# Kernel optimization log

Measured on AMD Instinct MI355X. Metric: run time of the kernel, lower is better.

Reference implementation:

```python
import jax, jax.numpy as jnp
import numpy as np

E = 256        # emb_size
H = 8          # num_heads
D = E // H     # head_dim = 32
FF = 3 * E     # 768
NE = 6         # num_experts
TOPK = 2
EPS = 1e-6


def rotate_half(x):
    x1 = x[..., ::2]
    x2 = x[..., 1::2]
    return jnp.stack((-x2, x1), axis=-1).reshape(x.shape)


def rope_cos_sin(seq_len):
    inv_freq = 1.0 / (10000.0 ** (jnp.arange(0, D, 2, dtype=jnp.float32) / D))
    pos = jnp.arange(seq_len, dtype=jnp.float32)
    freqs = jnp.outer(pos, inv_freq)              # [S, D/2]
    emb = jnp.concatenate([freqs, freqs], axis=-1)  # [S, D]
    return jnp.cos(emb)[None, None], jnp.sin(emb)[None, None]


def rmsnorm(x, w):
    rms = jax.lax.rsqrt(jnp.mean(x * x, axis=-1, keepdims=True) + EPS)
    return x * rms * w


def setup_inputs() -> dict:
    key = jax.random.key(0)
    ks = jax.random.split(key, 10)
    s = lambda fan_in: 1.0 / np.sqrt(fan_in)
    return {
        "x": jax.random.normal(ks[0], (4, 2048, E), dtype=jnp.float32),
        "Wqkv": jax.random.uniform(ks[1], (E, 3 * E), jnp.float32, -s(E), s(E)),
        "Wout": jax.random.uniform(ks[2], (E, E), jnp.float32, -s(E), s(E)),
        "rms1_w": jnp.ones((E,), jnp.float32),
        "rms2_w": jnp.ones((E,), jnp.float32),
        "gate_W": jax.random.uniform(ks[3], (E, NE), jnp.float32, -s(E), s(E)),
        "Wg": jax.random.uniform(ks[4], (NE, E, FF), jnp.float32, -s(E), s(E)),
        "Wu": jax.random.uniform(ks[5], (NE, E, FF), jnp.float32, -s(E), s(E)),
        "Wd": jax.random.uniform(ks[6], (NE, FF, E), jnp.float32, -s(FF), s(FF)),
    }


def attention(xn, Wqkv, Wout):
    B, S, _ = xn.shape
    qkv = (xn @ Wqkv).reshape(B, S, 3, H, D).transpose(2, 0, 3, 1, 4)  # [3,B,H,S,D]
    q, k, v = qkv[0], qkv[1], qkv[2]
    cos, sin = rope_cos_sin(S)
    q = q * cos + rotate_half(q) * sin
    k = k * cos + rotate_half(k) * sin
    scores = jnp.einsum("bhqd,bhkd->bhqk", q, k) * (D ** -0.5)
    causal = jnp.arange(S)[None, :] > jnp.arange(S)[:, None]
    scores = jnp.where(causal[None, None], -jnp.inf, scores)
    attn = jax.nn.softmax(scores, axis=-1)
    out = jnp.einsum("bhqk,bhkd->bhqd", attn, v)
    out = out.transpose(0, 2, 1, 3).reshape(B, S, E)
    return out @ Wout


def moe(xn, gate_W, Wg, Wu, Wd):
    B, S, _ = xn.shape
    N = B * S
    gate_weights = jax.nn.softmax(xn @ gate_W, axis=-1)          # [B,S,NE]
    topk_w, topk_i = jax.lax.top_k(gate_weights, TOPK)           # [B,S,K]
    topk_w = jax.nn.softmax(topk_w, axis=-1)
    xf = xn.reshape(N, E)
    idx = topk_i.reshape(N, TOPK)
    wts = topk_w.reshape(N, TOPK)
    # dense all-expert compute, as in the original
    expert_out = jnp.einsum("ntf,nfe->nte",
                            jax.nn.silu(jnp.einsum("te,nef->ntf", xf, Wg))
                            * jnp.einsum("te,nef->ntf", xf, Wu),
                            Wd)                                   # [NE, N, E]
    weighted_sel = jnp.zeros((N, NE), xf.dtype).at[jnp.arange(N)[:, None], idx].add(wts)
    out = jnp.einsum("nte,tn->te", expert_out, weighted_sel).reshape(B, S, E)
    # load balancing aux loss
    importance = gate_weights.mean(axis=(0, 1))                   # [NE]
    load = jnp.zeros((NE,), xf.dtype).at[idx.reshape(-1)].add(1.0) / N
    aux_loss = NE * jnp.sum(importance * load)
    return out, aux_loss


def reference(x, Wqkv, Wout, rms1_w, rms2_w, gate_W, Wg, Wu, Wd):
    attn_out = attention(rmsnorm(x, rms1_w), Wqkv, Wout)
    x = x + attn_out
    ff_out, aux_loss = moe(rmsnorm(x, rms2_w), gate_W, Wg, Wu, Wd)
    return x + ff_out, aux_loss
```

## Files before the change

kernel.cpp:

```cpp
#include <hip/hip_runtime.h>
#include <hip/hip_bf16.h>
#include <math.h>

#define NE 6

typedef __bf16 bf16x8 __attribute__((ext_vector_type(8)));
typedef float f32x4 __attribute__((ext_vector_type(4)));
typedef short short8 __attribute__((ext_vector_type(8)));

#define SWZ(row, kbyte) (((row) * 128) + ((kbyte) ^ (((row) & 7) << 4)))

static __device__ __forceinline__ short f2bf(float f) {
    __hip_bfloat16 h = __float2bfloat16(f);
    return __builtin_bit_cast(short, h);
}

static __device__ __forceinline__ float bf2f(short s) {
    return __bfloat162float(__builtin_bit_cast(__hip_bfloat16, s));
}

__global__ void rope_tables(float* __restrict__ ct, float* __restrict__ st) {
    int id = blockIdx.x * 256 + threadIdx.x;
    if (id >= 2048 * 16) return;
    int s = id >> 4, f = id & 15;
    float invf = expf(-logf(10000.0f) * (float)f / 16.0f);
    float ang = (float)s * invf;
    ct[id] = cosf(ang);
    st[id] = sinf(ang);
}

__global__ void rmsnorm_k(const float* __restrict__ x, const float* __restrict__ w,
                          float* __restrict__ o) {
    __shared__ float red[256];
    int n = blockIdx.x, t = threadIdx.x;
    float v = x[n * 256 + t];
    red[t] = v * v;
    __syncthreads();
    for (int s = 128; s > 0; s >>= 1) {
        if (t < s) red[t] += red[t + s];
        __syncthreads();
    }
    float rms = rsqrtf(red[0] / 256.0f + 1e-6f);
    o[n * 256 + t] = v * rms * w[t];
}

__global__ void rmsnorm_both(const float* __restrict__ x, const float* __restrict__ w,
                             float* __restrict__ o, short* __restrict__ obf) {
    __shared__ float red[256];
    int n = blockIdx.x, t = threadIdx.x;
    float v = x[n * 256 + t];
    red[t] = v * v;
    __syncthreads();
    for (int s = 128; s > 0; s >>= 1) {
        if (t < s) red[t] += red[t + s];
        __syncthreads();
    }
    float rms = rsqrtf(red[0] / 256.0f + 1e-6f);
    float val = v * rms * w[t];
    o[n * 256 + t] = val;
    obf[n * 256 + t] = f2bf(val);
}

__global__ __launch_bounds__(256) void transcvt_k(const float* __restrict__ src,
                                                  short* __restrict__ dst, int R, int C) {
    __shared__ short tile[32][33];
    const float* s = src + (size_t)blockIdx.z * R * C;
    short* d = dst + (size_t)blockIdx.z * R * C;
    int t = threadIdx.x;
    int c0 = blockIdx.x * 32, r0 = blockIdx.y * 32;
    int ci = t & 31, ri0 = t >> 5;
#pragma unroll
    for (int it = 0; it < 4; it++) {
        int ri = ri0 + it * 8;
        tile[ri][ci] = f2bf(s[(size_t)(r0 + ri) * C + c0 + ci]);
    }
    __syncthreads();
#pragma unroll
    for (int it = 0; it < 4; it++) {
        int rj = ri0 + it * 8;
        d[(size_t)(c0 + rj) * R + r0 + ci] = tile[ci][rj];
    }
}

__global__ __launch_bounds__(256) void gemm_qkv(const float* __restrict__ A,
                                                const float* __restrict__ W,
                                                float* __restrict__ Q, float* __restrict__ Kq,
                                                float* __restrict__ V) {
    __shared__ float As[16][64];
    __shared__ float Bs[16][64];
    int t = threadIdx.x;
    int m0 = blockIdx.y * 64, n0 = blockIdx.x * 64;
    float acc[4][4] = {};
    int am = t >> 2, ak = (t & 3) * 4;
    int bk = t >> 4, bn = (t & 15) * 4;
    int tm = (t & 15) * 4, tn = (t >> 4) * 4;
    for (int k0 = 0; k0 < 256; k0 += 16) {
        float4 av = *(const float4*)&A[(m0 + am) * 256 + k0 + ak];
        As[ak + 0][am] = av.x; As[ak + 1][am] = av.y; As[ak + 2][am] = av.z; As[ak + 3][am] = av.w;
        float4 bv = *(const float4*)&W[(k0 + bk) * 768 + n0 + bn];
        *(float4*)&Bs[bk][bn] = bv;
        __syncthreads();
#pragma unroll
        for (int kk = 0; kk < 16; kk++) {
            float4 a4 = *(float4*)&As[kk][tm];
            float4 b4 = *(float4*)&Bs[kk][tn];
            float a[4] = {a4.x, a4.y, a4.z, a4.w};
            float b[4] = {b4.x, b4.y, b4.z, b4.w};
#pragma unroll
            for (int i = 0; i < 4; i++)
#pragma unroll
                for (int j = 0; j < 4; j++) acc[i][j] += a[i] * b[j];
        }
        __syncthreads();
    }
    int part = n0 >> 8;
    float* dst = part == 0 ? Q : (part == 1 ? Kq : V);
#pragma unroll
    for (int i = 0; i < 4; i++) {
        int rowi = m0 + tm + i;
        int b = rowi >> 11, s = rowi & 2047;
#pragma unroll
        for (int j = 0; j < 4; j++) {
            int c = n0 + tn + j;
            int e = c & 255, h = e >> 5, d = e & 31;
            dst[(((size_t)(b * 8 + h)) * 2048 + s) * 32 + d] = acc[i][j];
        }
    }
}

__global__ void rope_k(float* __restrict__ Q, float* __restrict__ Kq,
                       const float* __restrict__ ct, const float* __restrict__ st) {
    int id = blockIdx.x * 256 + threadIdx.x;
    if (id >= 32 * 2048 * 16) return;
    int i = id & 15;
    int s = (id >> 4) & 2047;
    int bh = id >> 15;
    int base = (bh * 2048 + s) * 32 + 2 * i;
    int j0 = (2 * i) & 15;
    float c0 = ct[s * 16 + j0], s0 = st[s * 16 + j0];
    float c1 = ct[s * 16 + j0 + 1], s1 = st[s * 16 + j0 + 1];
    float2 q = *(float2*)&Q[base];
    float2 k = *(float2*)&Kq[base];
    float2 qo, ko;
    qo.x = q.x * c0 - q.y * s0;
    qo.y = q.y * c1 + q.x * s1;
    ko.x = k.x * c0 - k.y * s0;
    ko.y = k.y * c1 + k.x * s1;
    *(float2*)&Q[base] = qo;
    *(float2*)&Kq[base] = ko;
}

__global__ __launch_bounds__(256) void attn_k(const float* __restrict__ Q,
                                              const float* __restrict__ Kg,
                                              const float* __restrict__ Vg,
                                              float* __restrict__ ctx) {
    __shared__ float4 Kl[64][8];
    __shared__ float4 Vl[64][8];
    int bh = blockIdx.x;
    int qt = gridDim.y - 1 - blockIdx.y;
    int t = threadIdx.x;
    int sub = t & 3;
    int row = qt * 64 + (t >> 2);
    const float4* Qb = (const float4*)(Q + (size_t)bh * 2048 * 32);
    const float4* Kb = (const float4*)(Kg + (size_t)bh * 2048 * 32);
    const float4* Vb = (const float4*)(Vg + (size_t)bh * 2048 * 32);
    float4 q0 = Qb[row * 8 + sub * 2];
    float4 q1 = Qb[row * 8 + sub * 2 + 1];
    float4 o0 = {}, o1 = {};
    float m = -1e30f, l = 0.f;
    const float scale = 0.17677669529663687f;
    int ntile = qt + 1;
    float4* Klf = &Kl[0][0];
    float4* Vlf = &Vl[0][0];
    for (int kt = 0; kt < ntile; kt++) {
        int kbase = kt * 64;
        Klf[t] = Kb[kbase * 8 + t];
        Klf[t + 256] = Kb[kbase * 8 + t + 256];
        Vlf[t] = Vb[kbase * 8 + t];
        Vlf[t + 256] = Vb[kbase * 8 + t + 256];
        __syncthreads();
        int jmax = row - kbase + 1;
        if (jmax > 64) jmax = 64;
        for (int j = 0; j < jmax; j++) {
            float4 k0 = Kl[j][sub * 2];
            float4 k1 = Kl[j][sub * 2 + 1];
            float s = q0.x * k0.x + q0.y * k0.y + q0.z * k0.z + q0.w * k0.w +
                      q1.x * k1.x + q1.y * k1.y + q1.z * k1.z + q1.w * k1.w;
            s += __shfl_xor(s, 1);
            s += __shfl_xor(s, 2);
            s *= scale;
            if (s > m) {
                float r = __expf(m - s);
                o0.x *= r; o0.y *= r; o0.z *= r; o0.w *= r;
                o1.x *= r; o1.y *= r; o1.z *= r; o1.w *= r;
                l *= r;
                m = s;
            }
            float p = __expf(s - m);
            l += p;
            float4 v0 = Vl[j][sub * 2];
            float4 v1 = Vl[j][sub * 2 + 1];
            o0.x += p * v0.x; o0.y += p * v0.y; o0.z += p * v0.z; o0.w += p * v0.w;
            o1.x += p * v1.x; o1.y += p * v1.y; o1.z += p * v1.z; o1.w += p * v1.w;
        }
        __syncthreads();
    }
    float invl = 1.f / l;
    int b = bh >> 3, h = bh & 7;
    float4* cp = (float4*)(ctx + ((size_t)(b * 2048 + row)) * 256 + h * 32 + sub * 8);
    o0.x *= invl; o0.y *= invl; o0.z *= invl; o0.w *= invl;
    o1.x *= invl; o1.y *= invl; o1.z *= invl; o1.w *= invl;
    cp[0] = o0;
    cp[1] = o1;
}

__global__ __launch_bounds__(256) void gemm_out(const float* __restrict__ A,
                                                const float* __restrict__ W,
                                                const float* __restrict__ xres,
                                                float* __restrict__ x2) {
    __shared__ float As[16][64];
    __shared__ float Bs[16][64];
    int t = threadIdx.x;
    int m0 = blockIdx.y * 64, n0 = blockIdx.x * 64;
    float acc[4][4] = {};
    int am = t >> 2, ak = (t & 3) * 4;
    int bk = t >> 4, bn = (t & 15) * 4;
    int tm = (t & 15) * 4, tn = (t >> 4) * 4;
    for (int k0 = 0; k0 < 256; k0 += 16) {
        float4 av = *(const float4*)&A[(m0 + am) * 256 + k0 + ak];
        As[ak + 0][am] = av.x; As[ak + 1][am] = av.y; As[ak + 2][am] = av.z; As[ak + 3][am] = av.w;
        float4 bv = *(const float4*)&W[(k0 + bk) * 256 + n0 + bn];
        *(float4*)&Bs[bk][bn] = bv;
        __syncthreads();
#pragma unroll
        for (int kk = 0; kk < 16; kk++) {
            float4 a4 = *(float4*)&As[kk][tm];
            float4 b4 = *(float4*)&Bs[kk][tn];
            float a[4] = {a4.x, a4.y, a4.z, a4.w};
            float b[4] = {b4.x, b4.y, b4.z, b4.w};
#pragma unroll
            for (int i = 0; i < 4; i++)
#pragma unroll
                for (int j = 0; j < 4; j++) acc[i][j] += a[i] * b[j];
        }
        __syncthreads();
    }
#pragma unroll
    for (int i = 0; i < 4; i++) {
        int rowi = m0 + tm + i;
#pragma unroll
        for (int j = 0; j < 4; j++) {
            int c = n0 + tn + j;
            x2[rowi * 256 + c] = acc[i][j] + xres[rowi * 256 + c];
        }
    }
}

__global__ void gate_k(const float* __restrict__ xn2, const float* __restrict__ gw,
                       int* __restrict__ idx, float* __restrict__ wts,
                       int* __restrict__ cnt, float* __restrict__ imp) {
    __shared__ float simp[NE];
    __shared__ int scnt[NE];
    int t = threadIdx.x;
    int n = blockIdx.x * 256 + t;
    if (t < NE) { simp[t] = 0.f; scnt[t] = 0; }
    __syncthreads();
    float lg[NE] = {0, 0, 0, 0, 0, 0};
    for (int k = 0; k < 256; k++) {
        float xv = xn2[n * 256 + k];
#pragma unroll
        for (int e = 0; e < NE; e++) lg[e] += xv * gw[k * NE + e];
    }
    float mx = lg[0];
#pragma unroll
    for (int e = 1; e < NE; e++) mx = fmaxf(mx, lg[e]);
    float p[NE], se = 0.f;
#pragma unroll
    for (int e = 0; e < NE; e++) { p[e] = expf(lg[e] - mx); se += p[e]; }
    float inv = 1.f / se;
#pragma unroll
    for (int e = 0; e < NE; e++) p[e] *= inv;
    int i1 = 0; float v1 = p[0];
#pragma unroll
    for (int e = 1; e < NE; e++) if (p[e] > v1) { v1 = p[e]; i1 = e; }
    int i2 = -1; float v2 = -1.f;
#pragma unroll
    for (int e = 0; e < NE; e++) if (e != i1 && p[e] > v2) { v2 = p[e]; i2 = e; }
    float e2v = expf(v2 - v1);
    float w1 = 1.f / (1.f + e2v);
    float w2 = e2v / (1.f + e2v);
    idx[n * 2] = i1; idx[n * 2 + 1] = i2;
    wts[n * 2] = w1; wts[n * 2 + 1] = w2;
#pragma unroll
    for (int e = 0; e < NE; e++) atomicAdd(&simp[e], p[e]);
    atomicAdd(&scnt[i1], 1);
    atomicAdd(&scnt[i2], 1);
    __syncthreads();
    if (t < NE) {
        atomicAdd(&imp[t], simp[t]);
        atomicAdd(&cnt[t], scnt[t]);
    }
}

__global__ void prefix_k(const int* __restrict__ cnt, const float* __restrict__ imp,
                         int* __restrict__ offs, int* __restrict__ cur,
                         float* __restrict__ auxout) {
    if (threadIdx.x == 0) {
        int o = 0;
        float a = 0.f;
        for (int e = 0; e < NE; e++) {
            offs[e] = o;
            cur[e] = o;
            o += cnt[e];
            a += imp[e] * (float)cnt[e];
        }
        auxout[0] = 6.0f * a / (8192.0f * 8192.0f);
    }
}

__global__ void scatter_k(const int* __restrict__ idx, int* __restrict__ cur,
                          int* __restrict__ ltok, int* __restrict__ slotp) {
    int n = blockIdx.x * 256 + threadIdx.x;
#pragma unroll
    for (int s = 0; s < 2; s++) {
        int e = idx[n * 2 + s];
        int pos = atomicAdd(&cur[e], 1);
        ltok[pos] = n;
        slotp[n * 2 + s] = pos;
    }
}

__global__ __launch_bounds__(256) void mfma_moe1(const short* __restrict__ xnbf,
                                                 const short* __restrict__ WgT,
                                                 const short* __restrict__ WuT,
                                                 const int* __restrict__ cnt,
                                                 const int* __restrict__ offs,
                                                 const int* __restrict__ ltok,
                                                 short* __restrict__ Hbuf) {
    int e = blockIdx.z;
    int Me = cnt[e];
    int m0 = blockIdx.y * 64;
    if (m0 >= Me) return;
    int off = offs[e];
    __shared__ short As[4096], Bg[4096], Bu[4096];
    __shared__ int stok[64];
    int t = threadIdx.x;
    if (t < 64) stok[t] = (m0 + t < Me) ? ltok[off + m0 + t] : ltok[off];
    __syncthreads();
    int n0 = blockIdx.x * 64;
    const short* WgE = WgT + (size_t)e * 768 * 256;
    const short* WuE = WuT + (size_t)e * 768 * 256;
    int lane = t & 63, wid = t >> 6, wr = wid >> 1, wc = wid & 1;
    int l15 = lane & 15, lh = lane >> 4;
    int r = t >> 3, k8 = (t & 7) * 8, kb8 = (t & 7) * 16;
    char* AsC = (char*)As; char* BgC = (char*)Bg; char* BuC = (char*)Bu;
    f32x4 accg[2][2] = {}, accu[2][2] = {};
    for (int k0 = 0; k0 < 256; k0 += 64) {
        short8 av0 = *(const short8*)&xnbf[(size_t)stok[r] * 256 + k0 + k8];
        short8 av1 = *(const short8*)&xnbf[(size_t)stok[r + 32] * 256 + k0 + k8];
        short8 gv0 = *(const short8*)&WgE[(size_t)(n0 + r) * 256 + k0 + k8];
        short8 gv1 = *(const short8*)&WgE[(size_t)(n0 + r + 32) * 256 + k0 + k8];
        short8 uv0 = *(const short8*)&WuE[(size_t)(n0 + r) * 256 + k0 + k8];
        short8 uv1 = *(const short8*)&WuE[(size_t)(n0 + r + 32) * 256 + k0 + k8];
        *(short8*)(AsC + SWZ(r, kb8)) = av0;
        *(short8*)(AsC + SWZ(r + 32, kb8)) = av1;
        *(short8*)(BgC + SWZ(r, kb8)) = gv0;
        *(short8*)(BgC + SWZ(r + 32, kb8)) = gv1;
        *(short8*)(BuC + SWZ(r, kb8)) = uv0;
        *(short8*)(BuC + SWZ(r + 32, kb8)) = uv1;
        __syncthreads();
#pragma unroll
        for (int kk = 0; kk < 2; kk++) {
            int kb = kk * 64 + lh * 16;
            bf16x8 a[2], bg[2], bu[2];
#pragma unroll
            for (int i = 0; i < 2; i++) {
                a[i]  = *(const bf16x8*)(AsC + SWZ(wr * 32 + i * 16 + l15, kb));
                bg[i] = *(const bf16x8*)(BgC + SWZ(wc * 32 + i * 16 + l15, kb));
                bu[i] = *(const bf16x8*)(BuC + SWZ(wc * 32 + i * 16 + l15, kb));
            }
#pragma unroll
            for (int mi = 0; mi < 2; mi++)
#pragma unroll
                for (int ni = 0; ni < 2; ni++) {
                    accg[mi][ni] = __builtin_amdgcn_mfma_f32_16x16x32_bf16(a[mi], bg[ni], accg[mi][ni], 0, 0, 0);
                    accu[mi][ni] = __builtin_amdgcn_mfma_f32_16x16x32_bf16(a[mi], bu[ni], accu[mi][ni], 0, 0, 0);
                }
        }
        __syncthreads();
    }
#pragma unroll
    for (int mi = 0; mi < 2; mi++)
#pragma unroll
        for (int j = 0; j < 4; j++) {
            int m = m0 + wr * 32 + mi * 16 + lh * 4 + j;
            if (m < Me) {
                size_t rp = (size_t)(off + m) * 768;
#pragma unroll
                for (int ni = 0; ni < 2; ni++) {
                    int c = n0 + wc * 32 + ni * 16 + l15;
                    float g = accg[mi][ni][j], u = accu[mi][ni][j];
                    Hbuf[rp + c] = f2bf(g / (1.f + __expf(-g)) * u);
                }
            }
        }
}

__global__ __launch_bounds__(256) void mfma_moe2(const short* __restrict__ Hbuf,
                                                 const short* __restrict__ WdT,
                                                 const int* __restrict__ cnt,
                                                 const int* __restrict__ offs,
                                                 short* __restrict__ Y) {
    int e = blockIdx.z;
    int Me = cnt[e];
    int m0 = blockIdx.y * 64;
    if (m0 >= Me) return;
    int off = offs[e];
    __shared__ short As[4096], Bs[4096];
    int t = threadIdx.x;
    int n0 = blockIdx.x * 64;
    const short* WdE = WdT + (size_t)e * 256 * 768;
    int lane = t & 63, wid = t >> 6, wr = wid >> 1, wc = wid & 1;
    int l15 = lane & 15, lh = lane >> 4;
    int r = t >> 3, k8 = (t & 7) * 8, kb8 = (t & 7) * 16;
    int ar0 = off + m0 + r;       if (ar0 > 16383) ar0 = 16383;
    int ar1 = off + m0 + r + 32;  if (ar1 > 16383) ar1 = 16383;
    char* AsC = (char*)As; char* BsC = (char*)Bs;
    f32x4 acc[2][2] = {};
    for (int k0 = 0; k0 < 768; k0 += 64) {
        short8 av0 = *(const short8*)&Hbuf[(size_t)ar0 * 768 + k0 + k8];
        short8 av1 = *(const short8*)&Hbuf[(size_t)ar1 * 768 + k0 + k8];
        short8 bv0 = *(const short8*)&WdE[(size_t)(n0 + r) * 768 + k0 + k8];
        short8 bv1 = *(const short8*)&WdE[(size_t)(n0 + r + 32) * 768 + k0 + k8];
        *(short8*)(AsC + SWZ(r, kb8)) = av0;
        *(short8*)(AsC + SWZ(r + 32, kb8)) = av1;
        *(short8*)(BsC + SWZ(r, kb8)) = bv0;
        *(short8*)(BsC + SWZ(r + 32, kb8)) = bv1;
        __syncthreads();
#pragma unroll
        for (int kk = 0; kk < 2; kk++) {
            int kb = kk * 64 + lh * 16;
            bf16x8 a[2], b[2];
#pragma unroll
            for (int i = 0; i < 2; i++) {
                a[i] = *(const bf16x8*)(AsC + SWZ(wr * 32 + i * 16 + l15, kb));
                b[i] = *(const bf16x8*)(BsC + SWZ(wc * 32 + i * 16 + l15, kb));
            }
#pragma unroll
            for (int mi = 0; mi < 2; mi++)
#pragma unroll
                for (int ni = 0; ni < 2; ni++)
                    acc[mi][ni] = __builtin_amdgcn_mfma_f32_16x16x32_bf16(a[mi], b[ni], acc[mi][ni], 0, 0, 0);
        }
        __syncthreads();
    }
#pragma unroll
    for (int mi = 0; mi < 2; mi++)
#pragma unroll
        for (int j = 0; j < 4; j++) {
            int m = m0 + wr * 32 + mi * 16 + lh * 4 + j;
            if (m < Me) {
                size_t rp = (size_t)(off + m) * 256;
#pragma unroll
                for (int ni = 0; ni < 2; ni++) {
                    int c = n0 + wc * 32 + ni * 16 + l15;
                    Y[rp + c] = f2bf(acc[mi][ni][j]);
                }
            }
        }
}

__global__ void combine_k(const float* __restrict__ x2, const short* __restrict__ Y,
                          const int* __restrict__ slotp, const float* __restrict__ wts,
                          float* __restrict__ out) {
    int n = blockIdx.x, t = threadIdx.x;
    int p0 = slotp[n * 2], p1 = slotp[n * 2 + 1];
    float w0 = wts[n * 2], w1 = wts[n * 2 + 1];
    out[n * 256 + t] = x2[n * 256 + t] + w0 * bf2f(Y[(size_t)p0 * 256 + t]) +
                       w1 * bf2f(Y[(size_t)p1 * 256 + t]);
}

extern "C" void kernel_launch(void* const* d_in, const int* in_sizes, int n_in,
                              void* d_out, int out_size, void* d_ws, size_t ws_size,
                              hipStream_t stream) {
    const float* x     = (const float*)d_in[0];
    const float* Wqkv  = (const float*)d_in[1];
    const float* Wout  = (const float*)d_in[2];
    const float* rms1w = (const float*)d_in[3];
    const float* rms2w = (const float*)d_in[4];
    const float* gateW = (const float*)d_in[5];
    const float* Wg    = (const float*)d_in[6];
    const float* Wu    = (const float*)d_in[7];
    const float* Wd    = (const float*)d_in[8];
    float* out = (float*)d_out;
    char* ws = (char*)d_ws;

    float* xn1   = (float*)(ws + 0);
    short* xn2bf = (short*)(ws + 0);
    float* Qb  = (float*)(ws + 8388608);
    float* Kb  = (float*)(ws + 16777216);
    float* Vb  = (float*)(ws + 25165824);
    short* Hbuf = (short*)(ws + 4194304);
    float* ctx = (float*)(ws + 33554432);
    short* WgT = (short*)(ws + 33554432);
    short* WuT = (short*)(ws + 35913728);
    short* WdT = (short*)(ws + 38273024);
    float* x2  = (float*)(ws + 41943040);
    float* xn2 = (float*)(ws + 50331648);
    short* Ybuf = (short*)(ws + 50331648);
    float* ct  = (float*)(ws + 58720256);
    float* st  = (float*)(ws + 58851328);
    int*   idx = (int*)(ws + 58982400);
    float* wts = (float*)(ws + 59047936);
    int* slotp = (int*)(ws + 59113472);
    int* ltok  = (int*)(ws + 59179008);
    int* cnt   = (int*)(ws + 59244544);
    int* offs  = cnt + 8;
    int* cur   = cnt + 16;
    float* imp = (float*)(cnt + 24);

    (void)hipMemsetAsync(cnt, 0, 128, stream);

    rope_tables<<<128, 256, 0, stream>>>(ct, st);
    rmsnorm_k<<<8192, 256, 0, stream>>>(x, rms1w, xn1);
    gemm_qkv<<<dim3(12, 128), 256, 0, stream>>>(xn1, Wqkv, Qb, Kb, Vb);
    rope_k<<<4096, 256, 0, stream>>>(Qb, Kb, ct, st);
    attn_k<<<dim3(32, 32), 256, 0, stream>>>(Qb, Kb, Vb, ctx);
    gemm_out<<<dim3(4, 128), 256, 0, stream>>>(ctx, Wout, x, x2);
    transcvt_k<<<dim3(24, 8, NE), 256, 0, stream>>>(Wg, WgT, 256, 768);
    transcvt_k<<<dim3(24, 8, NE), 256, 0, stream>>>(Wu, WuT, 256, 768);
    transcvt_k<<<dim3(8, 24, NE), 256, 0, stream>>>(Wd, WdT, 768, 256);
    rmsnorm_both<<<8192, 256, 0, stream>>>(x2, rms2w, xn2, xn2bf);
    gate_k<<<32, 256, 0, stream>>>(xn2, gateW, idx, wts, cnt, imp);
    prefix_k<<<1, 64, 0, stream>>>(cnt, imp, offs, cur, out + 2097152);
    scatter_k<<<32, 256, 0, stream>>>(idx, cur, ltok, slotp);
    mfma_moe1<<<dim3(12, 256, NE), 256, 0, stream>>>(xn2bf, WgT, WuT, cnt, offs, ltok, Hbuf);
    mfma_moe2<<<dim3(4, 256, NE), 256, 0, stream>>>(Hbuf, WdT, cnt, offs, Ybuf);
    combine_k<<<8192, 256, 0, stream>>>(x2, Ybuf, slotp, wts, out);
}
```

Measured before the change: 736.0 us.

## Use split-bf16 MFMA for QKV/out GEMMs and unroll attention inner loop by four

```diff
diff --git a/kernel.cpp b/kernel.cpp
--- a/kernel.cpp
+++ b/kernel.cpp
@@ -17,6 +17,11 @@
 
 static __device__ __forceinline__ float bf2f(short s) {
     return __bfloat162float(__builtin_bit_cast(__hip_bfloat16, s));
+}
+
+static __device__ __forceinline__ float dot8(float4 a0, float4 a1, float4 b0, float4 b1) {
+    return a0.x * b0.x + a0.y * b0.y + a0.z * b0.z + a0.w * b0.w +
+           a1.x * b1.x + a1.y * b1.y + a1.z * b1.z + a1.w * b1.w;
 }
 
 __global__ void rope_tables(float* __restrict__ ct, float* __restrict__ st) {
@@ -29,8 +34,8 @@
     st[id] = sinf(ang);
 }
 
-__global__ void rmsnorm_k(const float* __restrict__ x, const float* __restrict__ w,
-                          float* __restrict__ o) {
+__global__ void rmsnorm_hilo(const float* __restrict__ x, const float* __restrict__ w,
+                             short* __restrict__ ohi, short* __restrict__ olo) {
     __shared__ float red[256];
     int n = blockIdx.x, t = threadIdx.x;
     float v = x[n * 256 + t];
@@ -41,7 +46,10 @@
         __syncthreads();
     }
     float rms = rsqrtf(red[0] / 256.0f + 1e-6f);
-    o[n * 256 + t] = v * rms * w[t];
+    float val = v * rms * w[t];
+    short h = f2bf(val);
+    ohi[n * 256 + t] = h;
+    olo[n * 256 + t] = f2bf(val - bf2f(h));
 }
 
 __global__ void rmsnorm_both(const float* __restrict__ x, const float* __restrict__ w,
@@ -82,50 +90,167 @@
     }
 }
 
-__global__ __launch_bounds__(256) void gemm_qkv(const float* __restrict__ A,
-                                                const float* __restrict__ W,
-                                                float* __restrict__ Q, float* __restrict__ Kq,
-                                                float* __restrict__ V) {
-    __shared__ float As[16][64];
-    __shared__ float Bs[16][64];
+__global__ __launch_bounds__(256) void transcvt2_k(const float* __restrict__ src,
+                                                   short* __restrict__ dhi,
+                                                   short* __restrict__ dlo, int R, int C) {
+    __shared__ short th[32][33];
+    __shared__ short tl[32][33];
+    int t = threadIdx.x;
+    int c0 = blockIdx.x * 32, r0 = blockIdx.y * 32;
+    int ci = t & 31, ri0 = t >> 5;
+#pragma unroll
+    for (int it = 0; it < 4; it++) {
+        int ri = ri0 + it * 8;
+        float v = src[(size_t)(r0 + ri) * C + c0 + ci];
+        short h = f2bf(v);
+        th[ri][ci] = h;
+        tl[ri][ci] = f2bf(v - bf2f(h));
+    }
+    __syncthreads();
+#pragma unroll
+    for (int it = 0; it < 4; it++) {
+        int rj = ri0 + it * 8;
+        dhi[(size_t)(c0 + rj) * R + r0 + ci] = th[ci][rj];
+        dlo[(size_t)(c0 + rj) * R + r0 + ci] = tl[ci][rj];
+    }
+}
+
+__global__ __launch_bounds__(256) void mfma_qkv3(const short* __restrict__ Ahi,
+                                                 const short* __restrict__ Alo,
+                                                 const short* __restrict__ Bhi,
+                                                 const short* __restrict__ Blo,
+                                                 float* __restrict__ Q, float* __restrict__ Kq,
+                                                 float* __restrict__ V) {
+    __shared__ short sAh[4096], sAl[4096], sBh[4096], sBl[4096];
     int t = threadIdx.x;
     int m0 = blockIdx.y * 64, n0 = blockIdx.x * 64;
-    float acc[4][4] = {};
-    int am = t >> 2, ak = (t & 3) * 4;
-    int bk = t >> 4, bn = (t & 15) * 4;
-    int tm = (t & 15) * 4, tn = (t >> 4) * 4;
-    for (int k0 = 0; k0 < 256; k0 += 16) {
-        float4 av = *(const float4*)&A[(m0 + am) * 256 + k0 + ak];
-        As[ak + 0][am] = av.x; As[ak + 1][am] = av.y; As[ak + 2][am] = av.z; As[ak + 3][am] = av.w;
-        float4 bv = *(const float4*)&W[(k0 + bk) * 768 + n0 + bn];
-        *(float4*)&Bs[bk][bn] = bv;
-        __syncthreads();
-#pragma unroll
-        for (int kk = 0; kk < 16; kk++) {
-            float4 a4 = *(float4*)&As[kk][tm];
-            float4 b4 = *(float4*)&Bs[kk][tn];
-            float a[4] = {a4.x, a4.y, a4.z, a4.w};
-            float b[4] = {b4.x, b4.y, b4.z, b4.w};
-#pragma unroll
-            for (int i = 0; i < 4; i++)
-#pragma unroll
-                for (int j = 0; j < 4; j++) acc[i][j] += a[i] * b[j];
+    int lane = t & 63, wid = t >> 6, wr = wid >> 1, wc = wid & 1;
+    int l15 = lane & 15, lh = lane >> 4;
+    int r = t >> 3, k8 = (t & 7) * 8, kb8 = (t & 7) * 16;
+    char* Ah = (char*)sAh; char* Al = (char*)sAl; char* Bh = (char*)sBh; char* Bl = (char*)sBl;
+    f32x4 acc[2][2] = {};
+    for (int k0 = 0; k0 < 256; k0 += 64) {
+        short8 ah0 = *(const short8*)&Ahi[(size_t)(m0 + r) * 256 + k0 + k8];
+        short8 ah1 = *(const short8*)&Ahi[(size_t)(m0 + r + 32) * 256 + k0 + k8];
+        short8 al0 = *(const short8*)&Alo[(size_t)(m0 + r) * 256 + k0 + k8];
+        short8 al1 = *(const short8*)&Alo[(size_t)(m0 + r + 32) * 256 + k0 + k8];
+        short8 bh0 = *(const short8*)&Bhi[(size_t)(n0 + r) * 256 + k0 + k8];
+        short8 bh1 = *(const short8*)&Bhi[(size_t)(n0 + r + 32) * 256 + k0 + k8];
+        short8 bl0 = *(const short8*)&Blo[(size_t)(n0 + r) * 256 + k0 + k8];
+        short8 bl1 = *(const short8*)&Blo[(size_t)(n0 + r + 32) * 256 + k0 + k8];
+        *(short8*)(Ah + SWZ(r, kb8)) = ah0;
+        *(short8*)(Ah + SWZ(r + 32, kb8)) = ah1;
+        *(short8*)(Al + SWZ(r, kb8)) = al0;
+        *(short8*)(Al + SWZ(r + 32, kb8)) = al1;
+        *(short8*)(Bh + SWZ(r, kb8)) = bh0;
+        *(short8*)(Bh + SWZ(r + 32, kb8)) = bh1;
+        *(short8*)(Bl + SWZ(r, kb8)) = bl0;
+        *(short8*)(Bl + SWZ(r + 32, kb8)) = bl1;
+        __syncthreads();
+#pragma unroll
+        for (int kk = 0; kk < 2; kk++) {
+            int kb = kk * 64 + lh * 16;
+            bf16x8 ah[2], al[2], bh[2], bl[2];
+#pragma unroll
+            for (int i = 0; i < 2; i++) {
+                ah[i] = *(const bf16x8*)(Ah + SWZ(wr * 32 + i * 16 + l15, kb));
+                al[i] = *(const bf16x8*)(Al + SWZ(wr * 32 + i * 16 + l15, kb));
+                bh[i] = *(const bf16x8*)(Bh + SWZ(wc * 32 + i * 16 + l15, kb));
+                bl[i] = *(const bf16x8*)(Bl + SWZ(wc * 32 + i * 16 + l15, kb));
+            }
+#pragma unroll
+            for (int mi = 0; mi < 2; mi++)
+#pragma unroll
+                for (int ni = 0; ni < 2; ni++) {
+                    acc[mi][ni] = __builtin_amdgcn_mfma_f32_16x16x32_bf16(ah[mi], bh[ni], acc[mi][ni], 0, 0, 0);
+                    acc[mi][ni] = __builtin_amdgcn_mfma_f32_16x16x32_bf16(ah[mi], bl[ni], acc[mi][ni], 0, 0, 0);
+                    acc[mi][ni] = __builtin_amdgcn_mfma_f32_16x16x32_bf16(al[mi], bh[ni], acc[mi][ni], 0, 0, 0);
+                }
         }
         __syncthreads();
     }
     int part = n0 >> 8;
     float* dst = part == 0 ? Q : (part == 1 ? Kq : V);
 #pragma unroll
-    for (int i = 0; i < 4; i++) {
-        int rowi = m0 + tm + i;
-        int b = rowi >> 11, s = rowi & 2047;
+    for (int mi = 0; mi < 2; mi++)
 #pragma unroll
         for (int j = 0; j < 4; j++) {
-            int c = n0 + tn + j;
-            int e = c & 255, h = e >> 5, d = e & 31;
-            dst[(((size_t)(b * 8 + h)) * 2048 + s) * 32 + d] = acc[i][j];
-        }
-    }
+            int m = m0 + wr * 32 + mi * 16 + lh * 4 + j;
+            int b = m >> 11, s = m & 2047;
+#pragma unroll
+            for (int ni = 0; ni < 2; ni++) {
+                int c = n0 + wc * 32 + ni * 16 + l15;
+                int e = c & 255, h = e >> 5, d = e & 31;
+                dst[(((size_t)(b * 8 + h)) * 2048 + s) * 32 + d] = acc[mi][ni][j];
+            }
+        }
+}
+
+__global__ __launch_bounds__(256) void mfma_out3(const short* __restrict__ Ahi,
+                                                 const short* __restrict__ Alo,
+                                                 const short* __restrict__ Bhi,
+                                                 const short* __restrict__ Blo,
+                                                 const float* __restrict__ xres,
+                                                 float* __restrict__ x2) {
+    __shared__ short sAh[4096], sAl[4096], sBh[4096], sBl[4096];
+    int t = threadIdx.x;
+    int m0 = blockIdx.y * 64, n0 = blockIdx.x * 64;
+    int lane = t & 63, wid = t >> 6, wr = wid >> 1, wc = wid & 1;
+    int l15 = lane & 15, lh = lane >> 4;
+    int r = t >> 3, k8 = (t & 7) * 8, kb8 = (t & 7) * 16;
+    char* Ah = (char*)sAh; char* Al = (char*)sAl; char* Bh = (char*)sBh; char* Bl = (char*)sBl;
+    f32x4 acc[2][2] = {};
+    for (int k0 = 0; k0 < 256; k0 += 64) {
+        short8 ah0 = *(const short8*)&Ahi[(size_t)(m0 + r) * 256 + k0 + k8];
+        short8 ah1 = *(const short8*)&Ahi[(size_t)(m0 + r + 32) * 256 + k0 + k8];
+        short8 al0 = *(const short8*)&Alo[(size_t)(m0 + r) * 256 + k0 + k8];
+        short8 al1 = *(const short8*)&Alo[(size_t)(m0 + r + 32) * 256 + k0 + k8];
+        short8 bh0 = *(const short8*)&Bhi[(size_t)(n0 + r) * 256 + k0 + k8];
+        short8 bh1 = *(const short8*)&Bhi[(size_t)(n0 + r + 32) * 256 + k0 + k8];
+        short8 bl0 = *(const short8*)&Blo[(size_t)(n0 + r) * 256 + k0 + k8];
+        short8 bl1 = *(const short8*)&Blo[(size_t)(n0 + r + 32) * 256 + k0 + k8];
+        *(short8*)(Ah + SWZ(r, kb8)) = ah0;
+        *(short8*)(Ah + SWZ(r + 32, kb8)) = ah1;
+        *(short8*)(Al + SWZ(r, kb8)) = al0;
+        *(short8*)(Al + SWZ(r + 32, kb8)) = al1;
+        *(short8*)(Bh + SWZ(r, kb8)) = bh0;
+        *(short8*)(Bh + SWZ(r + 32, kb8)) = bh1;
+        *(short8*)(Bl + SWZ(r, kb8)) = bl0;
+        *(short8*)(Bl + SWZ(r + 32, kb8)) = bl1;
+        __syncthreads();
+#pragma unroll
+        for (int kk = 0; kk < 2; kk++) {
+            int kb = kk * 64 + lh * 16;
+            bf16x8 ah[2], al[2], bh[2], bl[2];
+#pragma unroll
+            for (int i = 0; i < 2; i++) {
+                ah[i] = *(const bf16x8*)(Ah + SWZ(wr * 32 + i * 16 + l15, kb));
+                al[i] = *(const bf16x8*)(Al + SWZ(wr * 32 + i * 16 + l15, kb));
+                bh[i] = *(const bf16x8*)(Bh + SWZ(wc * 32 + i * 16 + l15, kb));
+                bl[i] = *(const bf16x8*)(Bl + SWZ(wc * 32 + i * 16 + l15, kb));
+            }
+#pragma unroll
+            for (int mi = 0; mi < 2; mi++)
+#pragma unroll
+                for (int ni = 0; ni < 2; ni++) {
+                    acc[mi][ni] = __builtin_amdgcn_mfma_f32_16x16x32_bf16(ah[mi], bh[ni], acc[mi][ni], 0, 0, 0);
+                    acc[mi][ni] = __builtin_amdgcn_mfma_f32_16x16x32_bf16(ah[mi], bl[ni], acc[mi][ni], 0, 0, 0);
+                    acc[mi][ni] = __builtin_amdgcn_mfma_f32_16x16x32_bf16(al[mi], bh[ni], acc[mi][ni], 0, 0, 0);
+                }
+        }
+        __syncthreads();
+    }
+#pragma unroll
+    for (int mi = 0; mi < 2; mi++)
+#pragma unroll
+        for (int j = 0; j < 4; j++) {
+            int m = m0 + wr * 32 + mi * 16 + lh * 4 + j;
+#pragma unroll
+            for (int ni = 0; ni < 2; ni++) {
+                int c = n0 + wc * 32 + ni * 16 + l15;
+                x2[(size_t)m * 256 + c] = acc[mi][ni][j] + xres[(size_t)m * 256 + c];
+            }
+        }
 }
 
 __global__ void rope_k(float* __restrict__ Q, float* __restrict__ Kq,
@@ -153,7 +278,8 @@
 __global__ __launch_bounds__(256) void attn_k(const float* __restrict__ Q,
                                               const float* __restrict__ Kg,
                                               const float* __restrict__ Vg,
-                                              float* __restrict__ ctx) {
+                                              short* __restrict__ ctxh,
+                                              short* __restrict__ ctxl) {
     __shared__ float4 Kl[64][8];
     __shared__ float4 Vl[64][8];
     int bh = blockIdx.x;
@@ -181,79 +307,64 @@
         __syncthreads();
         int jmax = row - kbase + 1;
         if (jmax > 64) jmax = 64;
-        for (int j = 0; j < jmax; j++) {
-            float4 k0 = Kl[j][sub * 2];
-            float4 k1 = Kl[j][sub * 2 + 1];
-            float s = q0.x * k0.x + q0.y * k0.y + q0.z * k0.z + q0.w * k0.w +
-                      q1.x * k1.x + q1.y * k1.y + q1.z * k1.z + q1.w * k1.w;
-            s += __shfl_xor(s, 1);
-            s += __shfl_xor(s, 2);
-            s *= scale;
-            if (s > m) {
-                float r = __expf(m - s);
-                o0.x *= r; o0.y *= r; o0.z *= r; o0.w *= r;
-                o1.x *= r; o1.y *= r; o1.z *= r; o1.w *= r;
-                l *= r;
-                m = s;
-            }
-            float p = __expf(s - m);
-            l += p;
-            float4 v0 = Vl[j][sub * 2];
-            float4 v1 = Vl[j][sub * 2 + 1];
-            o0.x += p * v0.x; o0.y += p * v0.y; o0.z += p * v0.z; o0.w += p * v0.w;
-            o1.x += p * v1.x; o1.y += p * v1.y; o1.z += p * v1.z; o1.w += p * v1.w;
+        for (int j = 0; j < jmax; j += 4) {
+            int j1 = (j + 1) & 63, j2 = (j + 2) & 63, j3 = (j + 3) & 63;
+            float s0 = dot8(q0, q1, Kl[j][sub * 2], Kl[j][sub * 2 + 1]);
+            float s1 = dot8(q0, q1, Kl[j1][sub * 2], Kl[j1][sub * 2 + 1]);
+            float s2 = dot8(q0, q1, Kl[j2][sub * 2], Kl[j2][sub * 2 + 1]);
+            float s3 = dot8(q0, q1, Kl[j3][sub * 2], Kl[j3][sub * 2 + 1]);
+            s0 += __shfl_xor(s0, 1);
+            s1 += __shfl_xor(s1, 1);
+            s2 += __shfl_xor(s2, 1);
+            s3 += __shfl_xor(s3, 1);
+            s0 += __shfl_xor(s0, 2);
+            s1 += __shfl_xor(s1, 2);
+            s2 += __shfl_xor(s2, 2);
+            s3 += __shfl_xor(s3, 2);
+            s0 *= scale;
+            s1 *= scale;
+            s2 *= scale;
+            s3 *= scale;
+            s1 = (j + 1 < jmax) ? s1 : -1e30f;
+            s2 = (j + 2 < jmax) ? s2 : -1e30f;
+            s3 = (j + 3 < jmax) ? s3 : -1e30f;
+            float mn = fmaxf(m, fmaxf(fmaxf(s0, s1), fmaxf(s2, s3)));
+            float rr = __expf(m - mn);
+            float p0 = __expf(s0 - mn);
+            float p1 = __expf(s1 - mn);
+            float p2 = __expf(s2 - mn);
+            float p3 = __expf(s3 - mn);
+            l = l * rr + ((p0 + p1) + (p2 + p3));
+            float4 v00 = Vl[j][sub * 2],  v01 = Vl[j][sub * 2 + 1];
+            float4 v10 = Vl[j1][sub * 2], v11 = Vl[j1][sub * 2 + 1];
+            float4 v20 = Vl[j2][sub * 2], v21 = Vl[j2][sub * 2 + 1];
+            float4 v30 = Vl[j3][sub * 2], v31 = Vl[j3][sub * 2 + 1];
+            o0.x = o0.x * rr + p0 * v00.x + p1 * v10.x + p2 * v20.x + p3 * v30.x;
+            o0.y = o0.y * rr + p0 * v00.y + p1 * v10.y + p2 * v20.y + p3 * v30.y;
+            o0.z = o0.z * rr + p0 * v00.z + p1 * v10.z + p2 * v20.z + p3 * v30.z;
+            o0.w = o0.w * rr + p0 * v00.w + p1 * v10.w + p2 * v20.w + p3 * v30.w;
+            o1.x = o1.x * rr + p0 * v01.x + p1 * v11.x + p2 * v21.x + p3 * v31.x;
+            o1.y = o1.y * rr + p0 * v01.y + p1 * v11.y + p2 * v21.y + p3 * v31.y;
+            o1.z = o1.z * rr + p0 * v01.z + p1 * v11.z + p2 * v21.z + p3 * v31.z;
+            o1.w = o1.w * rr + p0 * v01.w + p1 * v11.w + p2 * v21.w + p3 * v31.w;
+            m = mn;
         }
         __syncthreads();
     }
     float invl = 1.f / l;
     int b = bh >> 3, h = bh & 7;
-    float4* cp = (float4*)(ctx + ((size_t)(b * 2048 + row)) * 256 + h * 32 + sub * 8);
-    o0.x *= invl; o0.y *= invl; o0.z *= invl; o0.w *= invl;
-    o1.x *= invl; o1.y *= invl; o1.z *= invl; o1.w *= invl;
-    cp[0] = o0;
-    cp[1] = o1;
-}
-
-__global__ __launch_bounds__(256) void gemm_out(const float* __restrict__ A,
-                                                const float* __restrict__ W,
-                                                const float* __restrict__ xres,
-                                                float* __restrict__ x2) {
-    __shared__ float As[16][64];
-    __shared__ float Bs[16][64];
-    int t = threadIdx.x;
-    int m0 = blockIdx.y * 64, n0 = blockIdx.x * 64;
-    float acc[4][4] = {};
-    int am = t >> 2, ak = (t & 3) * 4;
-    int bk = t >> 4, bn = (t & 15) * 4;
-    int tm = (t & 15) * 4, tn = (t >> 4) * 4;
-    for (int k0 = 0; k0 < 256; k0 += 16) {
-        float4 av = *(const float4*)&A[(m0 + am) * 256 + k0 + ak];
-        As[ak + 0][am] = av.x; As[ak + 1][am] = av.y; As[ak + 2][am] = av.z; As[ak + 3][am] = av.w;
-        float4 bv = *(const float4*)&W[(k0 + bk) * 256 + n0 + bn];
-        *(float4*)&Bs[bk][bn] = bv;
-        __syncthreads();
-#pragma unroll
-        for (int kk = 0; kk < 16; kk++) {
-            float4 a4 = *(float4*)&As[kk][tm];
-            float4 b4 = *(float4*)&Bs[kk][tn];
-            float a[4] = {a4.x, a4.y, a4.z, a4.w};
-            float b[4] = {b4.x, b4.y, b4.z, b4.w};
-#pragma unroll
-            for (int i = 0; i < 4; i++)
-#pragma unroll
-                for (int j = 0; j < 4; j++) acc[i][j] += a[i] * b[j];
-        }
-        __syncthreads();
-    }
-#pragma unroll
-    for (int i = 0; i < 4; i++) {
-        int rowi = m0 + tm + i;
-#pragma unroll
-        for (int j = 0; j < 4; j++) {
-            int c = n0 + tn + j;
-            x2[rowi * 256 + c] = acc[i][j] + xres[rowi * 256 + c];
-        }
-    }
+    float vals[8] = {o0.x * invl, o0.y * invl, o0.z * invl, o0.w * invl,
+                     o1.x * invl, o1.y * invl, o1.z * invl, o1.w * invl};
+    short8 hs, ls;
+#pragma unroll
+    for (int i = 0; i < 8; i++) {
+        short hv = f2bf(vals[i]);
+        hs[i] = hv;
+        ls[i] = f2bf(vals[i] - bf2f(hv));
+    }
+    size_t base = ((size_t)(b * 2048 + row)) * 256 + h * 32 + sub * 8;
+    *(short8*)&ctxh[base] = hs;
+    *(short8*)&ctxl[base] = ls;
 }
 
 __global__ void gate_k(const float* __restrict__ xn2, const float* __restrict__ gw,
@@ -495,18 +606,24 @@
     float* out = (float*)d_out;
     char* ws = (char*)d_ws;
 
-    float* xn1   = (float*)(ws + 0);
+    short* xn1hi = (short*)(ws + 0);
+    short* xn1lo = (short*)(ws + 4194304);
     short* xn2bf = (short*)(ws + 0);
     float* Qb  = (float*)(ws + 8388608);
     float* Kb  = (float*)(ws + 16777216);
     float* Vb  = (float*)(ws + 25165824);
     short* Hbuf = (short*)(ws + 4194304);
-    float* ctx = (float*)(ws + 33554432);
+    short* ctxh = (short*)(ws + 33554432);
+    short* ctxl = (short*)(ws + 37748736);
     short* WgT = (short*)(ws + 33554432);
     short* WuT = (short*)(ws + 35913728);
     short* WdT = (short*)(ws + 38273024);
     float* x2  = (float*)(ws + 41943040);
     float* xn2 = (float*)(ws + 50331648);
+    short* WqkvThi = (short*)(ws + 50331648);
+    short* WqkvTlo = (short*)(ws + 50724864);
+    short* WoutThi = (short*)(ws + 51118080);
+    short* WoutTlo = (short*)(ws + 51249152);
     short* Ybuf = (short*)(ws + 50331648);
     float* ct  = (float*)(ws + 58720256);
     float* st  = (float*)(ws + 58851328);
@@ -522,11 +639,13 @@
     (void)hipMemsetAsync(cnt, 0, 128, stream);
 
     rope_tables<<<128, 256, 0, stream>>>(ct, st);
-    rmsnorm_k<<<8192, 256, 0, stream>>>(x, rms1w, xn1);
-    gemm_qkv<<<dim3(12, 128), 256, 0, stream>>>(xn1, Wqkv, Qb, Kb, Vb);
+    transcvt2_k<<<dim3(24, 8), 256, 0, stream>>>(Wqkv, WqkvThi, WqkvTlo, 256, 768);
+    transcvt2_k<<<dim3(8, 8), 256, 0, stream>>>(Wout, WoutThi, WoutTlo, 256, 256);
+    rmsnorm_hilo<<<8192, 256, 0, stream>>>(x, rms1w, xn1hi, xn1lo);
+    mfma_qkv3<<<dim3(12, 128), 256, 0, stream>>>(xn1hi, xn1lo, WqkvThi, WqkvTlo, Qb, Kb, Vb);
     rope_k<<<4096, 256, 0, stream>>>(Qb, Kb, ct, st);
-    attn_k<<<dim3(32, 32), 256, 0, stream>>>(Qb, Kb, Vb, ctx);
-    gemm_out<<<dim3(4, 128), 256, 0, stream>>>(ctx, Wout, x, x2);
+    attn_k<<<dim3(32, 32), 256, 0, stream>>>(Qb, Kb, Vb, ctxh, ctxl);
+    mfma_out3<<<dim3(4, 128), 256, 0, stream>>>(ctxh, ctxl, WoutThi, WoutTlo, x, x2);
     transcvt_k<<<dim3(24, 8, NE), 256, 0, stream>>>(Wg, WgT, 256, 768);
     transcvt_k<<<dim3(24, 8, NE), 256, 0, stream>>>(Wu, WuT, 256, 768);
     transcvt_k<<<dim3(8, 24, NE), 256, 0, stream>>>(Wd, WdT, 768, 256);
```

Result: faster. 675.3 us (-8.2%).
